# Kernel tuning notes

Hardware: AMD Instinct MI355X
Metric: run time of the kernel (lower is better)

## Reference

```python
import jax, jax.numpy as jnp
import numpy as np

DIMENSIONS = 1000
NUM_LEVELS = 10
SIZE = 28
BATCH = 256
NUM_CLASSES = 10


def setup_inputs() -> dict:
    key = jax.random.key(0)
    k1, k2, k3 = jax.random.split(key, 3)
    # pixel values in [0, 1]
    x = jax.random.uniform(k1, (BATCH, SIZE, SIZE), dtype=jnp.float32)
    # fixed bipolar position hypervectors (bundle of x/y Level HVs); use +-1 like MAP HVs
    position = jnp.where(jax.random.normal(k2, (SIZE * SIZE, DIMENSIONS)) > 0, 1.0, -1.0).astype(jnp.float32)
    # Level value embedding table
    value_table = jnp.where(jax.random.normal(k3, (NUM_LEVELS, DIMENSIONS)) > 0, 1.0, -1.0).astype(jnp.float32)
    # classifier weight, initialized to zero in the original module
    W = jnp.zeros((NUM_CLASSES, DIMENSIONS), dtype=jnp.float32)
    return {"x": x, "position": position, "value_table": value_table, "W": W}


def reference(x, position, value_table, W):
    B = x.shape[0]
    xf = x.reshape(B, -1)  # [B, P] flatten
    # torchhd Level value_to_index with low=0, high=1
    idx = jnp.clip(jnp.round(xf * (NUM_LEVELS - 1)), 0, NUM_LEVELS - 1).astype(jnp.int32)
    hv = value_table[idx]                         # gather: [B, P, D]
    bound = position[None, :, :] * hv             # bind:   [B, P, D]
    s = jnp.sum(bound, axis=1)                    # multiset sum over pixels: [B, D]
    enc = jnp.where(s > 0, 1.0, -1.0).astype(x.dtype)  # hard_quantize
    logit = enc @ W.T                             # [B, num_classes]
    return logit
```

## Files before the change

### kernel.cpp

```cpp
#include <hip/hip_runtime.h>
#include <stdint.h>

#define DIMS   1000
#define NLEV   10
#define NPIX   784
#define NBATCH 256
#define NCLS   10
#define WPD    32
#define HALF   392

__global__ void pack_bits(const float* __restrict__ position,
                          const float* __restrict__ value_table,
                          uint32_t* __restrict__ ws_bits) {
    int i = blockIdx.x * blockDim.x + threadIdx.x;
    const int n_pos = NPIX * WPD;
    const int n_tot = n_pos + NLEV * WPD;
    if (i >= n_tot) return;
    const float* src;
    int row, w;
    if (i < n_pos) { row = i >> 5; w = i & 31; src = position; }
    else           { int k = i - n_pos; row = k >> 5; w = k & 31; src = value_table; }

    uint32_t bits = 0;
    const float4* s4 = (const float4*)(src + row * DIMS + w * 32);
    #pragma unroll
    for (int c = 0; c < 8; ++c) {
        int d = w * 32 + c * 4;
        if (d < DIMS) {
            float4 v = s4[c];
            bits |= (v.x > 0.f ? 1u : 0u) << (c * 4 + 0);
            bits |= (v.y > 0.f ? 1u : 0u) << (c * 4 + 1);
            bits |= (v.z > 0.f ? 1u : 0u) << (c * 4 + 2);
            bits |= (v.w > 0.f ? 1u : 0u) << (c * 4 + 3);
        }
    }
    ws_bits[i] = bits;
}

__global__ __launch_bounds__(256) void hdc_main(const float* __restrict__ x,
                                                const float* __restrict__ W,
                                                const uint32_t* __restrict__ ws_bits,
                                                float* __restrict__ out) {
    __shared__ alignas(16) uint32_t s_pos[HALF * WPD];
    __shared__ alignas(16) uint32_t s_vt[NLEV * WPD];
    __shared__ uint32_t s_idx[NPIX];
    __shared__ uint32_t s_cnt[32 * 8 * 7];
    __shared__ float    s_red[4][NCLS];

    const int b = blockIdx.x;
    const int t = threadIdx.x;

    for (int p = t; p < NPIX; p += 256) {
        float v = x[b * NPIX + p] * 9.0f;
        int l = (int)rintf(v);
        l = l < 0 ? 0 : (l > 9 ? 9 : l);
        s_idx[p] = (uint32_t)l;
    }
    {
        const uint4* src = (const uint4*)(ws_bits + NPIX * WPD);
        uint4* dst = (uint4*)s_vt;
        if (t < 80) dst[t] = src[t];
    }

    const int w = t & 31;
    const int g = t >> 5;
    uint32_t c0 = 0, c1 = 0, c2 = 0, c3 = 0, c4 = 0, c5 = 0, c6 = 0;

    #pragma unroll
    for (int h = 0; h < 2; ++h) {
        {
            const uint4* src = (const uint4*)(ws_bits + (size_t)h * HALF * WPD);
            uint4* dst = (uint4*)s_pos;
            for (int i = t; i < 3136; i += 256) dst[i] = src[i];
        }
        __syncthreads();
        const int pbase = g * 49;
        #pragma unroll 7
        for (int k = 0; k < 49; ++k) {
            int pl = pbase + k;
            uint32_t l = s_idx[h * HALF + pl];
            uint32_t bits = ~(s_pos[pl * WPD + w] ^ s_vt[l * WPD + w]);
            uint32_t carry = bits, tmp;
            tmp = c0 & carry; c0 ^= carry; carry = tmp;
            tmp = c1 & carry; c1 ^= carry; carry = tmp;
            tmp = c2 & carry; c2 ^= carry; carry = tmp;
            tmp = c3 & carry; c3 ^= carry; carry = tmp;
            tmp = c4 & carry; c4 ^= carry; carry = tmp;
            tmp = c5 & carry; c5 ^= carry; carry = tmp;
            c6 ^= carry;
        }
        __syncthreads();
    }

    {
        int base = (w * 8 + g) * 7;
        s_cnt[base + 0] = c0; s_cnt[base + 1] = c1; s_cnt[base + 2] = c2;
        s_cnt[base + 3] = c3; s_cnt[base + 4] = c4; s_cnt[base + 5] = c5;
        s_cnt[base + 6] = c6;
    }
    __syncthreads();

    float partial[NCLS];
    #pragma unroll
    for (int c = 0; c < NCLS; ++c) partial[c] = 0.f;

    if (t < 250) {
        float enc[4];
        #pragma unroll
        for (int j = 0; j < 4; ++j) {
            int d = 4 * t + j;
            int w2 = d >> 5, bit = d & 31;
            int cnt = 0;
            #pragma unroll
            for (int g2 = 0; g2 < 8; ++g2) {
                int base = (w2 * 8 + g2) * 7;
                #pragma unroll
                for (int i = 0; i < 7; ++i)
                    cnt += (int)((s_cnt[base + i] >> bit) & 1u) << i;
            }
            enc[j] = (cnt > 392) ? 1.0f : -1.0f;
        }
        #pragma unroll
        for (int c = 0; c < NCLS; ++c) {
            const float4* wv = (const float4*)(W + c * DIMS + 4 * t);
            float4 wl = *wv;
            partial[c] = enc[0] * wl.x + enc[1] * wl.y + enc[2] * wl.z + enc[3] * wl.w;
        }
    }

    #pragma unroll
    for (int c = 0; c < NCLS; ++c) {
        #pragma unroll
        for (int off = 32; off > 0; off >>= 1)
            partial[c] += __shfl_down(partial[c], off);
    }
    const int lane = t & 63, wid = t >> 6;
    if (lane == 0) {
        #pragma unroll
        for (int c = 0; c < NCLS; ++c) s_red[wid][c] = partial[c];
    }
    __syncthreads();
    if (t < NCLS)
        out[b * NCLS + t] = s_red[0][t] + s_red[1][t] + s_red[2][t] + s_red[3][t];
}

extern "C" void kernel_launch(void* const* d_in, const int* in_sizes, int n_in,
                              void* d_out, int out_size, void* d_ws, size_t ws_size,
                              hipStream_t stream) {
    const float* x        = (const float*)d_in[0];
    const float* position = (const float*)d_in[1];
    const float* vtab     = (const float*)d_in[2];
    const float* W        = (const float*)d_in[3];
    float* out            = (float*)d_out;
    uint32_t* ws_bits     = (uint32_t*)d_ws;

    const int n_words = NPIX * WPD + NLEV * WPD;
    pack_bits<<<(n_words + 255) / 256, 256, 0, stream>>>(position, vtab, ws_bits);
    hdc_main<<<NBATCH, 256, 0, stream>>>(x, W, ws_bits, out);
}
```

Measured before the change: 77.76 us.

## Double threads per block to 512 and stage position bits in quarters

Raises the block size to 512 threads so 16 pixel groups per dimension-word each accumulate about 49 pixels, instead of 8 groups accumulating 98. The 6-plane bit-sliced counters now suffice, and the shared position buffer shrinks to a quarter of the pixels per stage, which cuts LDS use and may allow more resident blocks. The cost is four stage-and-sync rounds instead of two, and a final popcount reduction that reads 16 groups per dimension. The goal is more parallelism per block with only 256 blocks launched.

```diff
diff --git a/kernel.cpp b/kernel.cpp
--- a/kernel.cpp
+++ b/kernel.cpp
@@ -7,7 +7,9 @@
 #define NBATCH 256
 #define NCLS   10
 #define WPD    32
-#define HALF   392
+#define QPIX   196
+#define NGRP   16
+#define NPLANE 6
 
 __global__ void pack_bits(const float* __restrict__ position,
                           const float* __restrict__ value_table,
@@ -37,20 +39,20 @@
     ws_bits[i] = bits;
 }
 
-__global__ __launch_bounds__(256) void hdc_main(const float* __restrict__ x,
+__global__ __launch_bounds__(512) void hdc_main(const float* __restrict__ x,
                                                 const float* __restrict__ W,
                                                 const uint32_t* __restrict__ ws_bits,
                                                 float* __restrict__ out) {
-    __shared__ alignas(16) uint32_t s_pos[HALF * WPD];
+    __shared__ alignas(16) uint32_t s_pos[QPIX * WPD];
     __shared__ alignas(16) uint32_t s_vt[NLEV * WPD];
     __shared__ uint32_t s_idx[NPIX];
-    __shared__ uint32_t s_cnt[32 * 8 * 7];
-    __shared__ float    s_red[4][NCLS];
+    __shared__ uint32_t s_cnt[WPD * NGRP * NPLANE];
+    __shared__ float    s_red[8][NCLS];
 
     const int b = blockIdx.x;
     const int t = threadIdx.x;
 
-    for (int p = t; p < NPIX; p += 256) {
+    for (int p = t; p < NPIX; p += 512) {
         float v = x[b * NPIX + p] * 9.0f;
         int l = (int)rintf(v);
         l = l < 0 ? 0 : (l > 9 ? 9 : l);
@@ -64,21 +66,21 @@
 
     const int w = t & 31;
     const int g = t >> 5;
-    uint32_t c0 = 0, c1 = 0, c2 = 0, c3 = 0, c4 = 0, c5 = 0, c6 = 0;
+    uint32_t c0 = 0, c1 = 0, c2 = 0, c3 = 0, c4 = 0, c5 = 0;
 
     #pragma unroll
-    for (int h = 0; h < 2; ++h) {
+    for (int q = 0; q < 4; ++q) {
         {
-            const uint4* src = (const uint4*)(ws_bits + (size_t)h * HALF * WPD);
+            const uint4* src = (const uint4*)(ws_bits + (size_t)q * QPIX * WPD);
             uint4* dst = (uint4*)s_pos;
-            for (int i = t; i < 3136; i += 256) dst[i] = src[i];
+            for (int i = t; i < 1568; i += 512) dst[i] = src[i];
         }
         __syncthreads();
-        const int pbase = g * 49;
-        #pragma unroll 7
-        for (int k = 0; k < 49; ++k) {
-            int pl = pbase + k;
-            uint32_t l = s_idx[h * HALF + pl];
+        const int npix = (g < 12) ? 12 : 13;
+        #pragma unroll 4
+        for (int k = 0; k < npix; ++k) {
+            int pl = (k < 12) ? (g + 16 * k) : (192 + (g - 12));
+            uint32_t l = s_idx[q * QPIX + pl];
             uint32_t bits = ~(s_pos[pl * WPD + w] ^ s_vt[l * WPD + w]);
             uint32_t carry = bits, tmp;
             tmp = c0 & carry; c0 ^= carry; carry = tmp;
@@ -86,17 +88,15 @@
             tmp = c2 & carry; c2 ^= carry; carry = tmp;
             tmp = c3 & carry; c3 ^= carry; carry = tmp;
             tmp = c4 & carry; c4 ^= carry; carry = tmp;
-            tmp = c5 & carry; c5 ^= carry; carry = tmp;
-            c6 ^= carry;
+            c5 ^= carry;
         }
         __syncthreads();
     }
 
     {
-        int base = (w * 8 + g) * 7;
+        int base = (w * NGRP + g) * NPLANE;
         s_cnt[base + 0] = c0; s_cnt[base + 1] = c1; s_cnt[base + 2] = c2;
         s_cnt[base + 3] = c3; s_cnt[base + 4] = c4; s_cnt[base + 5] = c5;
-        s_cnt[base + 6] = c6;
     }
     __syncthreads();
 
@@ -104,27 +104,27 @@
     #pragma unroll
     for (int c = 0; c < NCLS; ++c) partial[c] = 0.f;
 
-    if (t < 250) {
-        float enc[4];
+    if (t < 500) {
+        float enc[2];
         #pragma unroll
-        for (int j = 0; j < 4; ++j) {
-            int d = 4 * t + j;
+        for (int j = 0; j < 2; ++j) {
+            int d = 2 * t + j;
             int w2 = d >> 5, bit = d & 31;
             int cnt = 0;
             #pragma unroll
-            for (int g2 = 0; g2 < 8; ++g2) {
-                int base = (w2 * 8 + g2) * 7;
+            for (int g2 = 0; g2 < NGRP; ++g2) {
+                int base = (w2 * NGRP + g2) * NPLANE;
                 #pragma unroll
-                for (int i = 0; i < 7; ++i)
+                for (int i = 0; i < NPLANE; ++i)
                     cnt += (int)((s_cnt[base + i] >> bit) & 1u) << i;
             }
             enc[j] = (cnt > 392) ? 1.0f : -1.0f;
         }
         #pragma unroll
         for (int c = 0; c < NCLS; ++c) {
-            const float4* wv = (const float4*)(W + c * DIMS + 4 * t);
-            float4 wl = *wv;
-            partial[c] = enc[0] * wl.x + enc[1] * wl.y + enc[2] * wl.z + enc[3] * wl.w;
+            const float2* wv = (const float2*)(W + c * DIMS + 2 * t);
+            float2 wl = *wv;
+            partial[c] = enc[0] * wl.x + enc[1] * wl.y;
         }
     }
 
@@ -140,8 +140,12 @@
         for (int c = 0; c < NCLS; ++c) s_red[wid][c] = partial[c];
     }
     __syncthreads();
-    if (t < NCLS)
-        out[b * NCLS + t] = s_red[0][t] + s_red[1][t] + s_red[2][t] + s_red[3][t];
+    if (t < NCLS) {
+        float acc = 0.f;
+        #pragma unroll
+        for (int v = 0; v < 8; ++v) acc += s_red[v][t];
+        out[b * NCLS + t] = acc;
+    }
 }
 
 extern "C" void kernel_launch(void* const* d_in, const int* in_sizes, int n_in,
@@ -156,5 +160,5 @@
 
     const int n_words = NPIX * WPD + NLEV * WPD;
     pack_bits<<<(n_words + 255) / 256, 256, 0, stream>>>(position, vtab, ws_bits);
-    hdc_main<<<NBATCH, 256, 0, stream>>>(x, W, ws_bits, out);
+    hdc_main<<<NBATCH, 512, 0, stream>>>(x, W, ws_bits, out);
 }
```

Measured after the change: 74.93 us. -3.6%, faster.
